# Kernel tuning notes

Hardware: AMD Instinct MI355X
Metric: run time of the kernel (lower is better)

The kernel has to match this reference:

```python
import jax, jax.numpy as jnp
import numpy as np

B, T, E, NH = 2, 2048, 512, 8
HD = E // NH
SCALE = float(HD) ** -0.5


def setup_inputs() -> dict:
    key = jax.random.key(0)
    ks = jax.random.split(key, 7)
    s = 0.02
    return {
        "x": jax.random.normal(ks[0], (B, T, E), dtype=jnp.float32),
        "w_qkv": jax.random.normal(ks[1], (E, 3 * E), dtype=jnp.float32) * s,
        "b_qkv": jax.random.normal(ks[2], (3 * E,), dtype=jnp.float32) * s,
        "w_od": jax.random.normal(ks[3], (E, 2 * NH), dtype=jnp.float32) * s,
        "b_od": jax.random.normal(ks[4], (2 * NH,), dtype=jnp.float32) * s,
        "w_out": jax.random.normal(ks[5], (E, E), dtype=jnp.float32) * s,
        "b_out": jax.random.normal(ks[6], (E,), dtype=jnp.float32) * s,
    }


def _heads(t):  # (B,T,E) -> (B*NH, T, HD)
    return t.reshape(B, T, NH, HD).transpose(0, 2, 1, 3).reshape(B * NH, T, HD)


def _point_mask(idx, j):  # idx: (B*NH,T) float indices -> one-hot (B*NH,T,T)
    return (j[None, None, :] == idx[:, :, None]).astype(jnp.float32)


def reference(x, w_qkv, b_qkv, w_od, b_od, w_out, b_out):
    qkv = x @ w_qkv + b_qkv
    Q, K, V = jnp.split(qkv, 3, axis=-1)  # each (B,T,E)

    od = Q @ w_od + b_od  # (B,T,2*NH)
    offset, duration = jnp.split(od, 2, axis=-1)
    offset = jnp.tanh(offset) * T
    duration = jax.nn.sigmoid(duration) * T

    query_index = jnp.arange(T, dtype=x.dtype)[None, :, None]  # (1,T,1)
    anchor = query_index + offset  # (B,T,NH)
    # 'b t nh -> (b nh) t'
    anchor = anchor.transpose(0, 2, 1).reshape(B * NH, T)
    duration = duration.transpose(0, 2, 1).reshape(B * NH, T)

    start = anchor - duration
    end = anchor + duration
    bound_l = jnp.floor(start)
    bound_r = jnp.ceil(end)
    anchor_l = jnp.floor(anchor)
    anchor_r = anchor_l + 1.0

    j = jnp.arange(T, dtype=x.dtype)
    neg_bound_weight = (bound_l - start)[:, :, None] * _point_mask(bound_l, j) \
                     + (end - bound_r)[:, :, None] * _point_mask(bound_r, j)
    anchor_dist_l = anchor - anchor_l
    anchor_weight = anchor_dist_l[:, :, None] * _point_mask(anchor_r, j) \
                  + (1.0 - anchor_dist_l)[:, :, None] * _point_mask(anchor_l, j)
    point_weight = 1.0 + neg_bound_weight + anchor_weight  # (B*NH,T,T)

    # segment mask: True OUTSIDE [bound_l, bound_r]
    attn_mask = (j[None, None, :] < bound_l[:, :, None]) | (j[None, None, :] > bound_r[:, :, None])

    Qh, Kh, Vh = _heads(Q), _heads(K), _heads(V)  # (B*NH, T, HD)
    scores = jnp.einsum('bic,brc->bir', Qh, Kh) * SCALE * point_weight
    scores = jnp.where(attn_mask, jnp.asarray(-1e8, scores.dtype), scores)
    attn = jax.nn.softmax(scores, axis=-1)
    out = jnp.einsum('bir,brc->bic', attn, Vh)  # (B*NH,T,HD)
    out = out.reshape(B, NH, T, HD).transpose(0, 2, 1, 3).reshape(B, T, E)
    return out @ w_out + b_out
```

## Files before the change

kernel.cpp:

```cpp
#include <hip/hip_runtime.h>
#include <math.h>

typedef float vf4 __attribute__((ext_vector_type(4)));
typedef float f32x4 __attribute__((ext_vector_type(4)));
typedef short bf16x8 __attribute__((ext_vector_type(8)));
typedef short short4v __attribute__((ext_vector_type(4)));
typedef int int2v __attribute__((ext_vector_type(2)));
typedef int int4v __attribute__((ext_vector_type(4)));

constexpr int B = 2, T = 2048, E = 512, NH = 8, HD = 64;
constexpr int BH = B * NH;
constexpr int NT = BH * T;
constexpr int KSPLIT = 4;
constexpr float SCALE = 0.125f;
constexpr float LOG2E = 1.44269504088896f;
constexpr float QSC = SCALE * LOG2E;

static __device__ __forceinline__ short f2bf(float f) {
  unsigned u = __float_as_uint(f);
  unsigned r = (u + 0x7fffu + ((u >> 16) & 1u)) >> 16;
  return (short)r;
}
static __device__ __forceinline__ unsigned pk2bf(float a, float b) {
  unsigned lo = (unsigned)(unsigned short)f2bf(a);
  unsigned hi = (unsigned)(unsigned short)f2bf(b);
  return lo | (hi << 16);
}
static __device__ __forceinline__ unsigned pkhu(float a, float b) {
  unsigned ua = __float_as_uint(a) + 0x8000u;
  unsigned ub = __float_as_uint(b) + 0x8000u;
  return __builtin_amdgcn_perm(ub, ua, 0x07060302u);
}
#if __has_builtin(__builtin_amdgcn_exp2f)
#define EXP2F(x) __builtin_amdgcn_exp2f(x)
#else
#define EXP2F(x) exp2f(x)
#endif
static __device__ __forceinline__ float bf2f(short s) {
  return __uint_as_float(((unsigned)(unsigned short)s) << 16);
}

__global__ __launch_bounds__(256) void prep_all(
    const float* __restrict__ x, const float* __restrict__ w_qkv,
    const float* __restrict__ b_qkv, const float* __restrict__ w_od,
    const float* __restrict__ b_od,
    short* __restrict__ xb, short* __restrict__ wTq, short* __restrict__ wTo,
    const float* __restrict__ w_out, float* __restrict__ Wc,
    float* __restrict__ bc)
{
  __shared__ float sh[8464];
  const int bid = blockIdx.x;
  const int tid = threadIdx.x;

  if (bid < 2048) {
    int idx = (bid * 256 + tid) * 4;
    vf4 v = *(const vf4*)&x[idx];
    short4v o;
    o[0] = f2bf(v[0]); o[1] = f2bf(v[1]); o[2] = f2bf(v[2]); o[3] = f2bf(v[3]);
    *(short4v*)&xb[idx] = o;
  } else if (bid < 3072) {
    const float* w; short* wT; int N, t;
    if (bid < 2816) { t = bid - 2048; w = w_qkv; wT = wTq; N = 1536; }
    else            { t = bid - 2816; w = w_out; wT = wTo; N = 512; }
    float (*tt)[33] = (float(*)[33])sh;
    const int k0 = (t & 15) * 32;
    const int n0 = (t >> 4) * 32;
    const int c = tid & 31, r = tid >> 5;
#pragma unroll
    for (int p = 0; p < 4; ++p)
      tt[r + p * 8][c] = w[(size_t)(k0 + r + p * 8) * N + n0 + c];
    __syncthreads();
#pragma unroll
    for (int p = 0; p < 4; ++p)
      wT[(size_t)(n0 + r + p * 8) * 512 + k0 + c] = f2bf(tt[c][r + p * 8]);
  } else {
    float* Lod = sh;
    float (*pb)[17] = (float(*)[17])(sh + 8192);
    const int bx = bid - 3072;
#pragma unroll
    for (int p = 0; p < 8; ++p) {
      int idx = (p * 256 + tid) * 4;
      *(vf4*)&Lod[idx] = *(const vf4*)&w_od[idx];
    }
    __syncthreads();
    if (bx < 32) {
      const int k = bx * 16 + (tid >> 4);
      const int c = tid & 15;
      float s = 0.0f;
      for (int m = 0; m < E; m += 4) {
        vf4 wq = *(const vf4*)&w_qkv[(size_t)k * 1536 + m];
        s += wq[0] * Lod[(m + 0) * 16 + c] + wq[1] * Lod[(m + 1) * 16 + c]
           + wq[2] * Lod[(m + 2) * 16 + c] + wq[3] * Lod[(m + 3) * 16 + c];
      }
      Wc[k * 16 + c] = s;
    } else {
      const int c = tid & 15, seg = tid >> 4;
      float s = 0.0f;
      for (int m = seg * 32; m < seg * 32 + 32; ++m)
        s += b_qkv[m] * Lod[m * 16 + c];
      pb[seg][c] = s;
      __syncthreads();
      if (tid < 16) {
        float acc = b_od[tid];
#pragma unroll
        for (int g = 0; g < 16; ++g) acc += pb[g][tid];
        bc[tid] = acc;
      }
    }
  }
}

__global__ __launch_bounds__(256) void qkv_od(
    const short* __restrict__ xb, const short* __restrict__ wT,
    const float* __restrict__ bias, short* __restrict__ qkvb,
    short* __restrict__ Vtg,
    const float* __restrict__ x, const float* __restrict__ Wc,
    const float* __restrict__ bc, float* __restrict__ prm)
{
  __shared__ __align__(16) short smem_s[16896];
  const int bid = blockIdx.x;
  const int tid = threadIdx.x;

  if (bid < 768) {
    const int wave = tid >> 6, lane = tid & 63;
    const int quad = lane >> 4, l15 = lane & 15;
    const int wm = wave >> 1, wn = wave & 1;
    const int bx = bid % 24, by = bid / 24;
    const int m0 = by * 128, n0 = bx * 64;

    f32x4 acc[4][2];
#pragma unroll
    for (int mi = 0; mi < 4; ++mi)
#pragma unroll
      for (int ni = 0; ni < 2; ++ni) acc[mi][ni] = (f32x4){0, 0, 0, 0};

    const int sr = tid >> 1, sc = (tid & 1) * 16;
    const int br2 = tid >> 2, bk2 = (tid & 3) * 8;

#define QLD(R, K0) do {                                                   \
      R[0] = *(const bf16x8*)&xb[(size_t)(m0 + sr) * 512 + (K0) + sc];    \
      R[1] = *(const bf16x8*)&xb[(size_t)(m0 + sr) * 512 + (K0) + sc + 8];\
      R[2] = *(const bf16x8*)&wT[(size_t)(n0 + br2) * 512 + (K0) + bk2];  \
    } while (0)
#define QST(BUF, R) do {                                                  \
      short* As_ = smem_s + (BUF) * 7680;                                 \
      short* Bt_ = As_ + 5120;                                            \
      *(bf16x8*)&As_[sr * 40 + sc] = R[0];                                \
      *(bf16x8*)&As_[sr * 40 + sc + 8] = R[1];                            \
      *(bf16x8*)&Bt_[br2 * 40 + bk2] = R[2];                              \
    } while (0)
#define QMM(BUF) do {                                                     \
      const short* As_ = smem_s + (BUF) * 7680;                           \
      const short* Bt_ = As_ + 5120;                                      \
      bf16x8 aA[4], bB[2];                                                \
      for (int mi = 0; mi < 4; ++mi)                                      \
        aA[mi] = *(const bf16x8*)&As_[(wm * 64 + mi * 16 + l15) * 40 + quad * 8]; \
      for (int ni = 0; ni < 2; ++ni)                                      \
        bB[ni] = *(const bf16x8*)&Bt_[(wn * 32 + ni * 16 + l15) * 40 + quad * 8]; \
      for (int mi = 0; mi < 4; ++mi)                                      \
        for (int ni = 0; ni < 2; ++ni)                                    \
          acc[mi][ni] = __builtin_amdgcn_mfma_f32_16x16x32_bf16(          \
              aA[mi], bB[ni], acc[mi][ni], 0, 0, 0);                      \
    } while (0)

    bf16x8 rA[3], rB[3];
    QLD(rA, 0); QST(0, rA);
    QLD(rA, 32);
    __syncthreads();
#pragma unroll 1
    for (int k0 = 0; k0 < 512; k0 += 64) {
      if (k0 + 64 < 512) QLD(rB, k0 + 64);
      QMM(0);
      QST(1, rA);
      __syncthreads();
      if (k0 + 96 < 512) QLD(rA, k0 + 96);
      QMM(1);
      if (k0 + 64 < 512) { QST(0, rB); __syncthreads(); }
    }
#undef QLD
#undef QST
#undef QMM

#pragma unroll
    for (int mi = 0; mi < 4; ++mi)
#pragma unroll
      for (int ni = 0; ni < 2; ++ni) {
        const int col = n0 + wn * 32 + ni * 16 + l15;
        const int rowb = m0 + wm * 64 + mi * 16 + quad * 4;
        const float bs = bias[col];
        if (col < 1024) {
          const float qs = (col < 512) ? QSC : 1.0f;
#pragma unroll
          for (int r = 0; r < 4; ++r)
            qkvb[(size_t)(rowb + r) * 1536 + col] =
                f2bf((acc[mi][ni][r] + bs) * qs);
        } else {
          const int h = (col - 1024) >> 6, hd = col & 63;
          const int b = rowb >> 11, tt = rowb & 2047;
          int2v pk;
          pk[0] = (int)pk2bf(acc[mi][ni][0] + bs, acc[mi][ni][1] + bs);
          pk[1] = (int)pk2bf(acc[mi][ni][2] + bs, acc[mi][ni][3] + bs);
          *(int2v*)&Vtg[(size_t)(((b << 3) + h) * 64 + hd) * T + tt] = pk;
        }
      }
  } else {
    float* Lod = (float*)smem_s;
    float* ods = ((float*)smem_s) + 8192;
    const int obx = bid - 768;
#pragma unroll
    for (int p = 0; p < 8; ++p) {
      int idx = (p * 256 + tid) * 4;
      *(vf4*)&Lod[idx] = *(const vf4*)&Wc[idx];
    }
    __syncthreads();

    const int r = tid >> 4, c = tid & 15;
    const int row = obx * 16 + r;
    float sum = bc[c];
    const float* qr = x + (size_t)row * E;
    for (int k = 0; k < E; k += 4) {
      vf4 q = *(const vf4*)&qr[k];
      sum += q[0] * Lod[(k + 0) * 16 + c]
           + q[1] * Lod[(k + 1) * 16 + c]
           + q[2] * Lod[(k + 2) * 16 + c]
           + q[3] * Lod[(k + 3) * 16 + c];
    }
    ods[r * 16 + c] = sum;
    __syncthreads();

    if (tid < 128) {
      const int rr = tid >> 3, h = tid & 7;
      const int grow = obx * 16 + rr;
      const int b = grow / T, i = grow % T;
      float o = ods[rr * 16 + h];
      float d = ods[rr * 16 + h + 8];
      float offset   = tanhf(o) * (float)T;
      float duration = (float)T / (1.0f + expf(-d));
      float anchor = (float)i + offset;
      float start = anchor - duration;
      float end   = anchor + duration;
      float bl = floorf(start);
      float br = ceilf(end);
      float al = floorf(anchor);
      float wbl = bl - start;
      float wbr = end - br;
      float af  = anchor - al;
      float rsc = 1.0f;
      if (br < 0.0f || bl > (float)(T - 1)) {
        bl = 0.0f; br = (float)(T - 1);
        wbl = 0.0f; wbr = 0.0f; al = -5.0f; af = 0.0f;
        rsc = 0.0f;
      }
      int idx = (b * NH + h) * T + i;
      prm[0 * NT + idx] = bl;
      prm[1 * NT + idx] = br;
      prm[2 * NT + idx] = wbl;
      prm[3 * NT + idx] = wbr;
      prm[4 * NT + idx] = al;
      prm[5 * NT + idx] = af;
      prm[6 * NT + idx] = rsc;
    }
  }
}

__global__ __launch_bounds__(256, 4) void flash_attn_mfma6(
    const short* __restrict__ qkvb, const short* __restrict__ Vtg,
    const float* __restrict__ prm,
    short* __restrict__ Opart, float* __restrict__ lpart)
{
  __shared__ __align__(16) short Ks[2][64 * 72];
  __shared__ __align__(16) short Vt[2][64 * 72];
  __shared__ __align__(16) short Ps[4][16 * 72];
  __shared__ float u_s[8];

  const int tid = threadIdx.x;
  const int wave = tid >> 6, lane = tid & 63;
  const int quad = lane >> 4, l15 = lane & 15;
  const int qt = blockIdx.x, bh = blockIdx.y, ks = blockIdx.z;
  const int b = bh >> 3, h = bh & 7;
  const int i0 = qt * 64;
  const int i = i0 + wave * 16 + l15;

  const int pidx = bh * T + i;
  float blf = prm[0 * NT + pidx];
  float brf = prm[1 * NT + pidx];
  float wbl = prm[2 * NT + pidx];
  float wbr = prm[3 * NT + pidx];
  float alf = prm[4 * NT + pidx];
  float afr = prm[5 * NT + pidx];
  float rsc = prm[6 * NT + pidx];
  const int bli = (int)blf, widi = (int)brf - bli, ali = (int)alf;
  const unsigned widu = (unsigned)widi;
  const float a1 = 1.0f - afr;

  bf16x8 aQ0, aQ1;
  {
    size_t bq = (size_t)(b * T + i) * 1536 + h * 64;
    aQ0 = *(const bf16x8*)&qkvb[bq + quad * 8];
    aQ1 = *(const bf16x8*)&qkvb[bq + 32 + quad * 8];
    if (rsc == 0.0f) {
      bf16x8 z = {0, 0, 0, 0, 0, 0, 0, 0};
      aQ0 = z; aQ1 = z;
    }
  }

  float bmn = blf, bmx = brf;
#pragma unroll
  for (int d = 1; d < 64; d <<= 1) {
    bmn = fminf(bmn, __shfl_xor(bmn, d));
    bmx = fmaxf(bmx, __shfl_xor(bmx, d));
  }
  if (lane == 0) { u_s[wave * 2] = bmn; u_s[wave * 2 + 1] = bmx; }
  __syncthreads();
  bmn = fminf(fminf(u_s[0], u_s[2]), fminf(u_s[4], u_s[6]));
  bmx = fmaxf(fmaxf(u_s[1], u_s[3]), fmaxf(u_s[5], u_s[7]));
  const int ktlo = max(ks * 8, max(((int)bmn) >> 6, 0));
  const int kthi = min(ks * 8 + 7, min(((int)bmx) >> 6, T / 64 - 1));

  f32x4 o[4];
#pragma unroll
  for (int c = 0; c < 4; ++c) o[c] = (f32x4){0, 0, 0, 0};
  f32x4 lq = (f32x4){0, 0, 0, 0};
  const short BF1 = (short)0x3F80;
  const bf16x8 vone = {BF1, BF1, BF1, BF1, BF1, BF1, BF1, BF1};

  const int rq = tid >> 3, cb = (tid & 7) * 8;
  const short* kbase = qkvb + (size_t)b * T * 1536 + 512 + h * 64 + cb;
  const short* vbase = Vtg + (size_t)bh * 64 * T + cb;

#define FLD(R, KT) do { int j_ = (KT) * 64;                              \
    R[0] = *(const bf16x8*)&kbase[(size_t)(j_ + rq) * 1536];             \
    R[1] = *(const bf16x8*)&kbase[(size_t)(j_ + 32 + rq) * 1536];        \
    R[2] = *(const bf16x8*)&vbase[(size_t)rq * T + j_];                  \
    R[3] = *(const bf16x8*)&vbase[(size_t)(32 + rq) * T + j_];           \
  } while (0)
#define FST(BUF, R) do {                                                 \
    *(bf16x8*)&Ks[BUF][rq * 72 + cb] = R[0];                             \
    *(bf16x8*)&Ks[BUF][(32 + rq) * 72 + cb] = R[1];                      \
    *(bf16x8*)&Vt[BUF][rq * 72 + cb] = R[2];                             \
    *(bf16x8*)&Vt[BUF][(32 + rq) * 72 + cb] = R[3];                      \
  } while (0)

  auto compute = [&](int bufc, int ktc) {
    const int j0 = ktc * 64;
    const short* KsB = Ks[bufc];
    const short* VtB = Vt[bufc];

    f32x4 s[4];
#pragma unroll
    for (int nc = 0; nc < 4; ++nc) {
      const short* kb = &KsB[(nc * 16 + l15) * 72 + quad * 8];
      f32x4 a = (f32x4){0, 0, 0, 0};
      a = __builtin_amdgcn_mfma_f32_16x16x32_bf16(*(const bf16x8*)&kb[0],  aQ0, a, 0, 0, 0);
      a = __builtin_amdgcn_mfma_f32_16x16x32_bf16(*(const bf16x8*)&kb[32], aQ1, a, 0, 0, 0);
      s[nc] = a;
    }

    const int clean = (bli < j0) & (bli + widi > j0 + 63) &
                      ((ali > j0 + 63) | (ali + 1 < j0));
    if (__all(clean)) {
#pragma unroll
      for (int nc = 0; nc < 4; ++nc) {
        float p0 = EXP2F(s[nc][0]);
        float p1 = EXP2F(s[nc][1]);
        float p2 = EXP2F(s[nc][2]);
        float p3 = EXP2F(s[nc][3]);
        int2v pk;
        pk[0] = (int)pkhu(p0, p1);
        pk[1] = (int)pkhu(p2, p3);
        *(int2v*)&Ps[wave][l15 * 72 + nc * 16 + quad * 4] = pk;
      }
    } else {
      const int dq  = j0 + quad * 4 - bli;
      const int dq2 = j0 + quad * 4 - ali;
#pragma unroll
      for (int nc = 0; nc < 4; ++nc) {
        const int dn = dq + nc * 16, d2n = dq2 + nc * 16;
        float pr[4];
#pragma unroll
        for (int r = 0; r < 4; ++r) {
          int d = dn + r, d2 = d2n + r;
          float e  = (d == 0) ? wbl : ((d == widi) ? wbr : 0.0f);
          float aw = (d2 == 0) ? a1 : ((d2 == 1) ? afr : 0.0f);
          float w = 1.0f + e + aw;
          float v = s[nc][r] * w;
          v = ((unsigned)d <= widu) ? v : -115.0f;
          pr[r] = EXP2F(v);
        }
        int2v pk;
        pk[0] = (int)pkhu(pr[0], pr[1]);
        pk[1] = (int)pkhu(pr[2], pr[3]);
        *(int2v*)&Ps[wave][l15 * 72 + nc * 16 + quad * 4] = pk;
      }
    }

    bf16x8 bP0 = *(const bf16x8*)&Ps[wave][l15 * 72 + quad * 8];
    bf16x8 bP1 = *(const bf16x8*)&Ps[wave][l15 * 72 + 32 + quad * 8];
    lq = __builtin_amdgcn_mfma_f32_16x16x32_bf16(vone, bP0, lq, 0, 0, 0);
    lq = __builtin_amdgcn_mfma_f32_16x16x32_bf16(vone, bP1, lq, 0, 0, 0);
#pragma unroll
    for (int nc2 = 0; nc2 < 4; ++nc2) {
      const short* vb = &VtB[(nc2 * 16 + l15) * 72 + quad * 8];
      o[nc2] = __builtin_amdgcn_mfma_f32_16x16x32_bf16(
          *(const bf16x8*)&vb[0],  bP0, o[nc2], 0, 0, 0);
      o[nc2] = __builtin_amdgcn_mfma_f32_16x16x32_bf16(
          *(const bf16x8*)&vb[32], bP1, o[nc2], 0, 0, 0);
    }
  };

  if (ktlo <= kthi) {
    bf16x8 rA[4], rB[4];
    FLD(rA, ktlo);
    FST(0, rA);
    if (ktlo + 1 <= kthi) FLD(rA, ktlo + 1);
    __syncthreads();
    int buf = 0, kt = ktlo;
    while (true) {
      if (kt + 2 <= kthi) FLD(rB, kt + 2);
      compute(buf, kt);
      if (kt == kthi) break;
      FST(buf ^ 1, rA);
      __syncthreads();
      buf ^= 1; ++kt;
      if (kt + 2 <= kthi) FLD(rA, kt + 2);
      compute(buf, kt);
      if (kt == kthi) break;
      FST(buf ^ 1, rB);
      __syncthreads();
      buf ^= 1; ++kt;
    }
  }
#undef FLD
#undef FST

  if (lane < 16)
    lpart[ks * NT + bh * T + i] = lq[0];

  size_t ob = (size_t)ks * (B * T * E) + (size_t)(b * T + i) * E + h * 64;
#pragma unroll
  for (int nc2 = 0; nc2 < 4; ++nc2) {
    int2v pk;
    pk[0] = (int)pk2bf(o[nc2][0], o[nc2][1]);
    pk[1] = (int)pk2bf(o[nc2][2], o[nc2][3]);
    *(int2v*)&Opart[ob + nc2 * 16 + quad * 4] = pk;
  }
}

__global__ __launch_bounds__(256) void combine_attn(
    const short* __restrict__ Opart, const float* __restrict__ lpart,
    short* __restrict__ attnb)
{
  int base = (blockIdx.x * 256 + threadIdx.x) * 8;
  int row = base >> 9;
  int c = base & 511;
  int h = c >> 6;
  int b = row >> 11;
  int i = row & (T - 1);
  int lidx = ((b << 3) + h) * T + i;
  float l = (lpart[lidx] + lpart[NT + lidx]) +
            (lpart[2 * NT + lidx] + lpart[3 * NT + lidx]);
  float inv = 1.0f / l;
  bf16x8 o0 = *(const bf16x8*)&Opart[base];
  bf16x8 o1 = *(const bf16x8*)&Opart[(size_t)(B * T * E) + base];
  bf16x8 o2 = *(const bf16x8*)&Opart[(size_t)(2 * B * T * E) + base];
  bf16x8 o3 = *(const bf16x8*)&Opart[(size_t)(3 * B * T * E) + base];
  int4v ov;
#pragma unroll
  for (int j = 0; j < 4; ++j) {
    float a = ((bf2f(o0[2 * j]) + bf2f(o1[2 * j])) +
               (bf2f(o2[2 * j]) + bf2f(o3[2 * j]))) * inv;
    float bb = ((bf2f(o0[2 * j + 1]) + bf2f(o1[2 * j + 1])) +
                (bf2f(o2[2 * j + 1]) + bf2f(o3[2 * j + 1]))) * inv;
    ov[j] = (int)pk2bf(a, bb);
  }
  *(int4v*)&attnb[base] = ov;
}

__global__ __launch_bounds__(256) void out_gemm_bf16(
    const short* __restrict__ Ab, const short* __restrict__ wT,
    const float* __restrict__ bias, float* __restrict__ Co)
{
  __shared__ __align__(16) short smem_o[10240];

  const int tid = threadIdx.x;
  const int wave = tid >> 6, lane = tid & 63;
  const int quad = lane >> 4, l15 = lane & 15;
  const int wm = wave >> 1, wn = wave & 1;
  const int m0 = blockIdx.y * 64, n0 = blockIdx.x * 64;

  f32x4 acc[2][2];
#pragma unroll
  for (int mi = 0; mi < 2; ++mi)
#pragma unroll
    for (int ni = 0; ni < 2; ++ni) acc[mi][ni] = (f32x4){0, 0, 0, 0};

  const int ar = tid >> 2, akc = (tid & 3) * 8;

#define OLD(R, K0) do {                                                  \
    R[0] = *(const bf16x8*)&Ab[(size_t)(m0 + ar) * 512 + (K0) + akc];    \
    R[1] = *(const bf16x8*)&wT[(size_t)(n0 + ar) * 512 + (K0) + akc];    \
  } while (0)
#define OST(BUF, R) do {                                                 \
    short* As_ = smem_o + (BUF) * 5120;                                  \
    short* Bt_ = As_ + 2560;                                             \
    *(bf16x8*)&As_[ar * 40 + akc] = R[0];                                \
    *(bf16x8*)&Bt_[ar * 40 + akc] = R[1];                                \
  } while (0)
#define OMM(BUF) do {                                                    \
    const short* As_ = smem_o + (BUF) * 5120;                            \
    const short* Bt_ = As_ + 2560;                                       \
    bf16x8 aA[2], bB[2];                                                 \
    for (int mi = 0; mi < 2; ++mi)                                       \
      aA[mi] = *(const bf16x8*)&As_[(wm * 32 + mi * 16 + l15) * 40 + quad * 8]; \
    for (int ni = 0; ni < 2; ++ni)                                       \
      bB[ni] = *(const bf16x8*)&Bt_[(wn * 32 + ni * 16 + l15) * 40 + quad * 8]; \
    for (int mi = 0; mi < 2; ++mi)                                       \
      for (int ni = 0; ni < 2; ++ni)                                     \
        acc[mi][ni] = __builtin_amdgcn_mfma_f32_16x16x32_bf16(           \
            aA[mi], bB[ni], acc[mi][ni], 0, 0, 0);                       \
  } while (0)

  bf16x8 rA[2], rB[2];
  OLD(rA, 0); OST(0, rA);
  OLD(rA, 32);
  __syncthreads();
#pragma unroll 1
  for (int k0 = 0; k0 < 512; k0 += 64) {
    if (k0 + 64 < 512) OLD(rB, k0 + 64);
    OMM(0);
    OST(1, rA);
    __syncthreads();
    if (k0 + 96 < 512) OLD(rA, k0 + 96);
    OMM(1);
    if (k0 + 64 < 512) { OST(0, rB); __syncthreads(); }
  }
#undef OLD
#undef OST
#undef OMM

#pragma unroll
  for (int mi = 0; mi < 2; ++mi)
#pragma unroll
    for (int ni = 0; ni < 2; ++ni)
#pragma unroll
      for (int r = 0; r < 4; ++r) {
        int row = m0 + wm * 32 + mi * 16 + quad * 4 + r;
        int col = n0 + wn * 32 + ni * 16 + l15;
        Co[(size_t)row * 512 + col] = acc[mi][ni][r] + bias[col];
      }
}

extern "C" void kernel_launch(void* const* d_in, const int* in_sizes, int n_in,
                              void* d_out, int out_size, void* d_ws, size_t ws_size,
                              hipStream_t stream)
{
  const float* x     = (const float*)d_in[0];
  const float* w_qkv = (const float*)d_in[1];
  const float* b_qkv = (const float*)d_in[2];
  const float* w_od  = (const float*)d_in[3];
  const float* b_od  = (const float*)d_in[4];
  const float* w_out = (const float*)d_in[5];
  const float* b_out = (const float*)d_in[6];
  float* out = (float*)d_out;

  char* w = (char*)d_ws;
  short* xb    = (short*)w;  w += (size_t)B * T * E * 2;
  short* wTq   = (short*)w;  w += (size_t)E * 3 * E * 2;
  short* wTo   = (short*)w;  w += (size_t)E * E * 2;
  short* qkvb  = (short*)w;  w += (size_t)B * T * 3 * E * 2;
  short* Vtg   = (short*)w;  w += (size_t)B * T * E * 2;
  float* Wc    = (float*)w;  w += (size_t)E * 16 * 4;
  float* bc    = (float*)w;  w += 256;
  float* prm   = (float*)w;  w += (size_t)7 * NT * 4;
  short* Opart = (short*)w;  w += (size_t)KSPLIT * B * T * E * 2;
  float* lpart = (float*)w;  w += (size_t)KSPLIT * NT * 4;
  short* attnb = (short*)w;  w += (size_t)B * T * E * 2;

  prep_all<<<dim3(3105), 256, 0, stream>>>(
      x, w_qkv, b_qkv, w_od, b_od, xb, wTq, wTo, w_out, Wc, bc);

  qkv_od<<<dim3(1024), 256, 0, stream>>>(
      xb, wTq, b_qkv, qkvb, Vtg, x, Wc, bc, prm);

  flash_attn_mfma6<<<dim3(T / 64, BH, KSPLIT), 256, 0, stream>>>(
      qkvb, Vtg, prm, Opart, lpart);

  combine_attn<<<dim3(B * T * E / 2048), 256, 0, stream>>>(Opart, lpart, attnb);

  out_gemm_bf16<<<dim3(E / 64, B * T / 64), 256, 0, stream>>>(
      attnb, wTo, b_out, out);
}
```

Measured before the change: 203.0 us.

## Widen QKV GEMM tiles and simplify flash-attn pipeline with scalar row sums

The QKV GEMM moves from 128x64 to 128x128 tiles, halving its block count (384 GEMM blocks instead of 768) and increasing register accumulators per wave. The flash attention kernel replaces the two-stage register prefetch with a simpler single-prefetch double-buffered loop. The MFMA-based row-sum of P is replaced by scalar accumulation of the unrounded fp32 probabilities plus a cross-quad shuffle reduction. Larger tiles raise reuse but add register pressure and reduce parallelism, and the shallower prefetch may expose more load latency.

```diff
diff --git a/kernel.cpp b/kernel.cpp
--- a/kernel.cpp
+++ b/kernel.cpp
@@ -117,53 +117,54 @@
     const float* __restrict__ x, const float* __restrict__ Wc,
     const float* __restrict__ bc, float* __restrict__ prm)
 {
-  __shared__ __align__(16) short smem_s[16896];
+  __shared__ __align__(16) short smem_s[20480];
   const int bid = blockIdx.x;
   const int tid = threadIdx.x;
 
-  if (bid < 768) {
+  if (bid < 384) {
     const int wave = tid >> 6, lane = tid & 63;
     const int quad = lane >> 4, l15 = lane & 15;
     const int wm = wave >> 1, wn = wave & 1;
-    const int bx = bid % 24, by = bid / 24;
-    const int m0 = by * 128, n0 = bx * 64;
-
-    f32x4 acc[4][2];
+    const int bx = bid % 12, by = bid / 12;
+    const int m0 = by * 128, n0 = bx * 128;
+
+    f32x4 acc[4][4];
 #pragma unroll
     for (int mi = 0; mi < 4; ++mi)
 #pragma unroll
-      for (int ni = 0; ni < 2; ++ni) acc[mi][ni] = (f32x4){0, 0, 0, 0};
+      for (int ni = 0; ni < 4; ++ni) acc[mi][ni] = (f32x4){0, 0, 0, 0};
 
     const int sr = tid >> 1, sc = (tid & 1) * 16;
-    const int br2 = tid >> 2, bk2 = (tid & 3) * 8;
 
 #define QLD(R, K0) do {                                                   \
       R[0] = *(const bf16x8*)&xb[(size_t)(m0 + sr) * 512 + (K0) + sc];    \
       R[1] = *(const bf16x8*)&xb[(size_t)(m0 + sr) * 512 + (K0) + sc + 8];\
-      R[2] = *(const bf16x8*)&wT[(size_t)(n0 + br2) * 512 + (K0) + bk2];  \
+      R[2] = *(const bf16x8*)&wT[(size_t)(n0 + sr) * 512 + (K0) + sc];    \
+      R[3] = *(const bf16x8*)&wT[(size_t)(n0 + sr) * 512 + (K0) + sc + 8];\
     } while (0)
 #define QST(BUF, R) do {                                                  \
-      short* As_ = smem_s + (BUF) * 7680;                                 \
+      short* As_ = smem_s + (BUF) * 10240;                                \
       short* Bt_ = As_ + 5120;                                            \
       *(bf16x8*)&As_[sr * 40 + sc] = R[0];                                \
       *(bf16x8*)&As_[sr * 40 + sc + 8] = R[1];                            \
-      *(bf16x8*)&Bt_[br2 * 40 + bk2] = R[2];                              \
+      *(bf16x8*)&Bt_[sr * 40 + sc] = R[2];                                \
+      *(bf16x8*)&Bt_[sr * 40 + sc + 8] = R[3];                            \
     } while (0)
 #define QMM(BUF) do {                                                     \
-      const short* As_ = smem_s + (BUF) * 7680;                           \
+      const short* As_ = smem_s + (BUF) * 10240;                          \
       const short* Bt_ = As_ + 5120;                                      \
-      bf16x8 aA[4], bB[2];                                                \
+      bf16x8 aA[4], bB[4];                                                \
       for (int mi = 0; mi < 4; ++mi)                                      \
         aA[mi] = *(const bf16x8*)&As_[(wm * 64 + mi * 16 + l15) * 40 + quad * 8]; \
-      for (int ni = 0; ni < 2; ++ni)                                      \
-        bB[ni] = *(const bf16x8*)&Bt_[(wn * 32 + ni * 16 + l15) * 40 + quad * 8]; \
+      for (int ni = 0; ni < 4; ++ni)                                      \
+        bB[ni] = *(const bf16x8*)&Bt_[(wn * 64 + ni * 16 + l15) * 40 + quad * 8]; \
       for (int mi = 0; mi < 4; ++mi)                                      \
-        for (int ni = 0; ni < 2; ++ni)                                    \
+        for (int ni = 0; ni < 4; ++ni)                                    \
           acc[mi][ni] = __builtin_amdgcn_mfma_f32_16x16x32_bf16(          \
               aA[mi], bB[ni], acc[mi][ni], 0, 0, 0);                      \
     } while (0)
 
-    bf16x8 rA[3], rB[3];
+    bf16x8 rA[4], rB[4];
     QLD(rA, 0); QST(0, rA);
     QLD(rA, 32);
     __syncthreads();
@@ -184,8 +185,8 @@
 #pragma unroll
     for (int mi = 0; mi < 4; ++mi)
 #pragma unroll
-      for (int ni = 0; ni < 2; ++ni) {
-        const int col = n0 + wn * 32 + ni * 16 + l15;
+      for (int ni = 0; ni < 4; ++ni) {
+        const int col = n0 + wn * 64 + ni * 16 + l15;
         const int rowb = m0 + wm * 64 + mi * 16 + quad * 4;
         const float bs = bias[col];
         if (col < 1024) {
@@ -206,7 +207,7 @@
   } else {
     float* Lod = (float*)smem_s;
     float* ods = ((float*)smem_s) + 8192;
-    const int obx = bid - 768;
+    const int obx = bid - 384;
 #pragma unroll
     for (int p = 0; p < 8; ++p) {
       int idx = (p * 256 + tid) * 4;
@@ -263,7 +264,7 @@
   }
 }
 
-__global__ __launch_bounds__(256, 4) void flash_attn_mfma6(
+__global__ __launch_bounds__(256, 4) void flash_attn_mfma5(
     const short* __restrict__ qkvb, const short* __restrict__ Vtg,
     const float* __restrict__ prm,
     short* __restrict__ Opart, float* __restrict__ lpart)
@@ -320,31 +321,40 @@
   f32x4 o[4];
 #pragma unroll
   for (int c = 0; c < 4; ++c) o[c] = (f32x4){0, 0, 0, 0};
-  f32x4 lq = (f32x4){0, 0, 0, 0};
-  const short BF1 = (short)0x3F80;
-  const bf16x8 vone = {BF1, BF1, BF1, BF1, BF1, BF1, BF1, BF1};
+  float lacc = 0.0f;
 
   const int rq = tid >> 3, cb = (tid & 7) * 8;
   const short* kbase = qkvb + (size_t)b * T * 1536 + 512 + h * 64 + cb;
   const short* vbase = Vtg + (size_t)bh * 64 * T + cb;
 
-#define FLD(R, KT) do { int j_ = (KT) * 64;                              \
-    R[0] = *(const bf16x8*)&kbase[(size_t)(j_ + rq) * 1536];             \
-    R[1] = *(const bf16x8*)&kbase[(size_t)(j_ + 32 + rq) * 1536];        \
-    R[2] = *(const bf16x8*)&vbase[(size_t)rq * T + j_];                  \
-    R[3] = *(const bf16x8*)&vbase[(size_t)(32 + rq) * T + j_];           \
-  } while (0)
-#define FST(BUF, R) do {                                                 \
-    *(bf16x8*)&Ks[BUF][rq * 72 + cb] = R[0];                             \
-    *(bf16x8*)&Ks[BUF][(32 + rq) * 72 + cb] = R[1];                      \
-    *(bf16x8*)&Vt[BUF][rq * 72 + cb] = R[2];                             \
-    *(bf16x8*)&Vt[BUF][(32 + rq) * 72 + cb] = R[3];                      \
-  } while (0)
-
-  auto compute = [&](int bufc, int ktc) {
-    const int j0 = ktc * 64;
-    const short* KsB = Ks[bufc];
-    const short* VtB = Vt[bufc];
+  bf16x8 kr0, kr1, vr0, vr1;
+  if (ktlo <= kthi) {
+    const int j0 = ktlo * 64;
+    kr0 = *(const bf16x8*)&kbase[(size_t)(j0 + rq) * 1536];
+    kr1 = *(const bf16x8*)&kbase[(size_t)(j0 + 32 + rq) * 1536];
+    vr0 = *(const bf16x8*)&vbase[(size_t)rq * T + j0];
+    vr1 = *(const bf16x8*)&vbase[(size_t)(32 + rq) * T + j0];
+    *(bf16x8*)&Ks[0][rq * 72 + cb] = kr0;
+    *(bf16x8*)&Ks[0][(32 + rq) * 72 + cb] = kr1;
+    *(bf16x8*)&Vt[0][rq * 72 + cb] = vr0;
+    *(bf16x8*)&Vt[0][(32 + rq) * 72 + cb] = vr1;
+  }
+  __syncthreads();
+
+  int buf = 0;
+#pragma unroll 1
+  for (int kt = ktlo; kt <= kthi; ++kt) {
+    const int j0 = kt * 64;
+    if (kt < kthi) {
+      const int j1 = j0 + 64;
+      kr0 = *(const bf16x8*)&kbase[(size_t)(j1 + rq) * 1536];
+      kr1 = *(const bf16x8*)&kbase[(size_t)(j1 + 32 + rq) * 1536];
+      vr0 = *(const bf16x8*)&vbase[(size_t)rq * T + j1];
+      vr1 = *(const bf16x8*)&vbase[(size_t)(32 + rq) * T + j1];
+    }
+
+    const short* KsB = Ks[buf];
+    const short* VtB = Vt[buf];
 
     f32x4 s[4];
 #pragma unroll
@@ -365,6 +375,7 @@
         float p1 = EXP2F(s[nc][1]);
         float p2 = EXP2F(s[nc][2]);
         float p3 = EXP2F(s[nc][3]);
+        lacc += (p0 + p1) + (p2 + p3);
         int2v pk;
         pk[0] = (int)pkhu(p0, p1);
         pk[1] = (int)pkhu(p2, p3);
@@ -385,7 +396,9 @@
           float w = 1.0f + e + aw;
           float v = s[nc][r] * w;
           v = ((unsigned)d <= widu) ? v : -115.0f;
-          pr[r] = EXP2F(v);
+          float p = EXP2F(v);
+          lacc += p;
+          pr[r] = p;
         }
         int2v pk;
         pk[0] = (int)pkhu(pr[0], pr[1]);
@@ -396,8 +409,6 @@
 
     bf16x8 bP0 = *(const bf16x8*)&Ps[wave][l15 * 72 + quad * 8];
     bf16x8 bP1 = *(const bf16x8*)&Ps[wave][l15 * 72 + 32 + quad * 8];
-    lq = __builtin_amdgcn_mfma_f32_16x16x32_bf16(vone, bP0, lq, 0, 0, 0);
-    lq = __builtin_amdgcn_mfma_f32_16x16x32_bf16(vone, bP1, lq, 0, 0, 0);
 #pragma unroll
     for (int nc2 = 0; nc2 < 4; ++nc2) {
       const short* vb = &VtB[(nc2 * 16 + l15) * 72 + quad * 8];
@@ -406,35 +417,23 @@
       o[nc2] = __builtin_amdgcn_mfma_f32_16x16x32_bf16(
           *(const bf16x8*)&vb[32], bP1, o[nc2], 0, 0, 0);
     }
-  };
-
-  if (ktlo <= kthi) {
-    bf16x8 rA[4], rB[4];
-    FLD(rA, ktlo);
-    FST(0, rA);
-    if (ktlo + 1 <= kthi) FLD(rA, ktlo + 1);
-    __syncthreads();
-    int buf = 0, kt = ktlo;
-    while (true) {
-      if (kt + 2 <= kthi) FLD(rB, kt + 2);
-      compute(buf, kt);
-      if (kt == kthi) break;
-      FST(buf ^ 1, rA);
+
+    if (kt < kthi) {
+      short* Kn = Ks[buf ^ 1];
+      short* Vn = Vt[buf ^ 1];
+      *(bf16x8*)&Kn[rq * 72 + cb] = kr0;
+      *(bf16x8*)&Kn[(32 + rq) * 72 + cb] = kr1;
+      *(bf16x8*)&Vn[rq * 72 + cb] = vr0;
+      *(bf16x8*)&Vn[(32 + rq) * 72 + cb] = vr1;
       __syncthreads();
-      buf ^= 1; ++kt;
-      if (kt + 2 <= kthi) FLD(rA, kt + 2);
-      compute(buf, kt);
-      if (kt == kthi) break;
-      FST(buf ^ 1, rB);
-      __syncthreads();
-      buf ^= 1; ++kt;
-    }
-  }
-#undef FLD
-#undef FST
-
+      buf ^= 1;
+    }
+  }
+
+  lacc += __shfl_xor(lacc, 16);
+  lacc += __shfl_xor(lacc, 32);
   if (lane < 16)
-    lpart[ks * NT + bh * T + i] = lq[0];
+    lpart[ks * NT + bh * T + i] = lacc;
 
   size_t ob = (size_t)ks * (B * T * E) + (size_t)(b * T + i) * E + h * 64;
 #pragma unroll
@@ -579,10 +578,10 @@
   prep_all<<<dim3(3105), 256, 0, stream>>>(
       x, w_qkv, b_qkv, w_od, b_od, xb, wTq, wTo, w_out, Wc, bc);
 
-  qkv_od<<<dim3(1024), 256, 0, stream>>>(
+  qkv_od<<<dim3(640), 256, 0, stream>>>(
       xb, wTq, b_qkv, qkvb, Vtg, x, Wc, bc, prm);
 
-  flash_attn_mfma6<<<dim3(T / 64, BH, KSPLIT), 256, 0, stream>>>(
+  flash_attn_mfma5<<<dim3(T / 64, BH, KSPLIT), 256, 0, stream>>>(
       qkvb, Vtg, prm, Opart, lpart);
 
   combine_attn<<<dim3(B * T * E / 2048), 256, 0, stream>>>(Opart, lpart, attnb);
```

Result: faster. 167.5 us (-17.5%).
